# Performance work log

Measured on AMD Instinct MI355X. Metric: run time of the kernel, lower is better.

Reference implementation:

```python
import jax, jax.numpy as jnp
import numpy as np

S, B, I, H, O = 2048, 4096, 1, 8, 1  # seq_len, batch, input_size, hidden_size, output_size


def setup_inputs() -> dict:
    key = jax.random.key(0)
    ks = jax.random.split(key, 11)
    bound = 1.0 / np.sqrt(H)  # torch LSTMCell/Linear default init range

    def p(k, shape):
        return jax.random.uniform(k, shape, jnp.float32, -bound, bound)

    return {
        "x": jax.random.normal(ks[0], (S, B, I), jnp.float32),
        "w_ih_f": p(ks[1], (4 * H, I)),
        "w_hh_f": p(ks[2], (4 * H, H)),
        "b_ih_f": p(ks[3], (4 * H,)),
        "b_hh_f": p(ks[4], (4 * H,)),
        "w_ih_b": p(ks[5], (4 * H, I)),
        "w_hh_b": p(ks[6], (4 * H, H)),
        "b_ih_b": p(ks[7], (4 * H,)),
        "b_hh_b": p(ks[8], (4 * H,)),
        "w_out": p(ks[9], (O, 2 * H)),
        "b_out": p(ks[10], (O,)),
        "future": 0,
    }


def _lstm_scan(xseq, w_ih, w_hh, b_ih, b_hh):
    """Run an LSTMCell (torch gate order i,f,g,o) over [S,B,I]; returns h seq [S,B,H]."""
    Sq, Bq, _ = xseq.shape
    Hq = w_hh.shape[1]
    # hoist the input projection out of the recurrence: one big GEMM
    xg = jnp.einsum('sbi,gi->sbg', xseq, w_ih) + b_ih + b_hh  # [S,B,4H]

    def step(carry, xg_t):
        h, c = carry
        gates = xg_t + h @ w_hh.T  # [B,4H]
        i_g, f_g, g_g, o_g = jnp.split(gates, 4, axis=-1)
        i_g = jax.nn.sigmoid(i_g)
        f_g = jax.nn.sigmoid(f_g)
        g_g = jnp.tanh(g_g)
        o_g = jax.nn.sigmoid(o_g)
        c = f_g * c + i_g * g_g
        h = o_g * jnp.tanh(c)
        return (h, c), h

    h0 = jnp.zeros((Bq, Hq), xseq.dtype)
    _, hs = jax.lax.scan(step, (h0, h0), xg)
    return hs


def reference(x, w_ih_f, w_hh_f, b_ih_f, b_hh_f, w_ih_b, w_hh_b, b_ih_b, b_hh_b, w_out, b_out, future):
    Sq, Bq, _ = x.shape
    # forward direction reads x[i]
    hf = _lstm_scan(x, w_ih_f, w_hh_f, b_ih_f, b_hh_f)  # [S,B,H]
    # backward cell reads x[future - i]; with torch negative indexing this is (future - i) mod S
    idx = (future - jnp.arange(Sq)) % Sq
    hb = _lstm_scan(x[idx], w_ih_b, w_hh_b, b_ih_b, b_hh_b)  # [S,B,H]
    # outputs[i] = Linear(cat(h_f[i], h_b[i]))
    h = jnp.concatenate([hf, hb], axis=-1)  # [S,B,2H]
    out = jnp.einsum('sbh,oh->sbo', h, w_out) + b_out  # [S,B,O]
    # torch.cat(outputs, dim=1): step-major columns -> [B, S*O]
    return out.transpose(1, 0, 2).reshape(Bq, Sq * out.shape[-1])
```

## Files before the change

### kernel.cpp

```cpp
#include <hip/hip_runtime.h>

#define SLEN  2048
#define BATCH 4096

template<int CTRL>
__device__ __forceinline__ float dppf(float v) {
#if __has_builtin(__builtin_amdgcn_mov_dpp)
    return __int_as_float(
        __builtin_amdgcn_mov_dpp(__float_as_int(v), CTRL, 0xF, 0xF, true));
#else
    return __int_as_float(
        __builtin_amdgcn_update_dpp(0, __float_as_int(v), CTRL, 0xF, 0xF, true));
#endif
}
#define DPP_XOR1 0xB1
#define DPP_XOR2 0x4E
#define DPP_XOR3 0x1B
#define DPP_XOR7 0x141

__device__ __forceinline__ void pkfma_acc(float2& acc, float2 a, float2 b) {
    asm("v_pk_fma_f32 %0, %1, %2, %0" : "+v"(acc) : "v"(a), "v"(b));
}
template<int Q>
__device__ __forceinline__ void pkfma_bc(float2& acc, float2 h2, float2 w) {
    if constexpr (Q == 0)
        asm("v_pk_fma_f32 %0, %1, %2, %0 op_sel:[0,0,0] op_sel_hi:[0,1,1]"
            : "+v"(acc) : "v"(h2), "v"(w));
    else
        asm("v_pk_fma_f32 %0, %1, %2, %0 op_sel:[1,0,0] op_sel_hi:[1,1,1]"
            : "+v"(acc) : "v"(h2), "v"(w));
}

extern "C" __global__ __launch_bounds__(256, 1)
void bilstm_kernel(const float* __restrict__ x,
                   const float* __restrict__ w_ih_f, const float* __restrict__ w_hh_f,
                   const float* __restrict__ b_ih_f, const float* __restrict__ b_hh_f,
                   const float* __restrict__ w_ih_b, const float* __restrict__ w_hh_b,
                   const float* __restrict__ b_ih_b, const float* __restrict__ b_hh_b,
                   const float* __restrict__ w_out, const float* __restrict__ b_out,
                   const int* __restrict__ future_p,
                   float* __restrict__ out)
{
    const int tid  = threadIdx.x;
    const int wv   = tid >> 6;
    const int lane = tid & 63;
    const int e    = lane >> 4;
    const int r    = lane & 15;
    const int d    = r >> 3;
    const int j    = r & 7;
    const int b    = blockIdx.x * 16 + wv * 4 + e;

    const float* wih_p = d ? w_ih_b : w_ih_f;
    const float* whh_p = d ? w_hh_b : w_hh_f;
    const float* bih_p = d ? b_ih_b : b_ih_f;
    const float* bhh_p = d ? b_hh_b : b_hh_f;

    const float SI = -1.4426950408889634f;
    const float SG = -2.8853900817779268f;

    const int M[8] = {0, 1, 2, 3, 7, 6, 5, 4};
    float2 Wif[8], Wgo[8], wih_if, wih_go, b_if, b_go;
    #pragma unroll
    for (int m = 0; m < 8; ++m) {
        const int idx = j ^ M[m];
        Wif[m].x = SI * whh_p[(0 + j) * 8 + idx];
        Wif[m].y = SI * whh_p[(8 + j) * 8 + idx];
        Wgo[m].x = SG * whh_p[(16 + j) * 8 + idx];
        Wgo[m].y = SI * whh_p[(24 + j) * 8 + idx];
    }
    wih_if.x = SI * wih_p[0 + j];   wih_if.y = SI * wih_p[8 + j];
    wih_go.x = SG * wih_p[16 + j];  wih_go.y = SI * wih_p[24 + j];
    b_if.x = SI * (bih_p[0 + j]  + bhh_p[0 + j]);
    b_if.y = SI * (bih_p[8 + j]  + bhh_p[8 + j]);
    b_go.x = SG * (bih_p[16 + j] + bhh_p[16 + j]);
    b_go.y = SI * (bih_p[24 + j] + bhh_p[24 + j]);

    const float wout = w_out[d * 8 + j];
    const float bout = b_out[0];
    const int   fut  = future_p[0];

    __shared__ float o_lds[4][4][2][33];

    float c  = 0.0f;
    float hn = 0.0f;

    const char* xb = (const char*)x;
    unsigned voff = ((unsigned)(d ? (fut & (SLEN - 1)) : 0) * BATCH + (unsigned)b) * 4u;
    const unsigned vdelta = d ? (unsigned)(-(BATCH * 4)) : (unsigned)(BATCH * 4);
    const unsigned vmask  = (unsigned)(SLEN * BATCH * 4 - 1);

    float xv[8], xn[8];
    #pragma unroll
    for (int u = 0; u < 8; ++u) {
        xv[u] = *(const float*)(xb + voff);
        voff = (voff + vdelta) & vmask;
    }

    for (int t0 = 0; t0 < SLEN; t0 += 8) {
        const bool pf = (t0 + 8) < SLEN;
        if (pf) {
            #pragma unroll
            for (int u = 0; u < 8; ++u) {
                xn[u] = *(const float*)(xb + voff);
                voff = (voff + vdelta) & vmask;
            }
        }
        #pragma unroll
        for (int u = 0; u < 8; ++u) {
            float2 P0, P1, P2, P3;
            P0.x = hn;
            P0.y = dppf<DPP_XOR1>(hn);
            P1.x = dppf<DPP_XOR2>(hn);
            P1.y = dppf<DPP_XOR3>(hn);
            P2.x = dppf<DPP_XOR7>(P0.x);
            P2.y = dppf<DPP_XOR7>(P0.y);
            P3.x = dppf<DPP_XOR7>(P1.x);
            P3.y = dppf<DPP_XOR7>(P1.y);

            float2 xv2; xv2.x = xv[u]; xv2.y = xv[u];
            float2 acc_if = b_if, acc_go = b_go;
            pkfma_acc(acc_if, xv2, wih_if);
            pkfma_acc(acc_go, xv2, wih_go);
            pkfma_bc<0>(acc_if, P0, Wif[0]);  pkfma_bc<1>(acc_if, P0, Wif[1]);
            pkfma_bc<0>(acc_if, P1, Wif[2]);  pkfma_bc<1>(acc_if, P1, Wif[3]);
            pkfma_bc<0>(acc_if, P2, Wif[4]);  pkfma_bc<1>(acc_if, P2, Wif[5]);
            pkfma_bc<0>(acc_if, P3, Wif[6]);  pkfma_bc<1>(acc_if, P3, Wif[7]);
            pkfma_bc<0>(acc_go, P0, Wgo[0]);  pkfma_bc<1>(acc_go, P0, Wgo[1]);
            pkfma_bc<0>(acc_go, P1, Wgo[2]);  pkfma_bc<1>(acc_go, P1, Wgo[3]);
            pkfma_bc<0>(acc_go, P2, Wgo[4]);  pkfma_bc<1>(acc_go, P2, Wgo[5]);
            pkfma_bc<0>(acc_go, P3, Wgo[6]);  pkfma_bc<1>(acc_go, P3, Wgo[7]);

            float ia = __builtin_amdgcn_rcpf(1.0f + __builtin_amdgcn_exp2f(acc_if.x));
            float fa = __builtin_amdgcn_rcpf(1.0f + __builtin_amdgcn_exp2f(acc_if.y));
            float rg = __builtin_amdgcn_rcpf(1.0f + __builtin_amdgcn_exp2f(acc_go.x));
            float oa = __builtin_amdgcn_rcpf(1.0f + __builtin_amdgcn_exp2f(acc_go.y));
            float ga = fmaf(2.0f, rg, -1.0f);

            c = fmaf(fa, c, ia * ga);
            float tc = __builtin_amdgcn_exp2f(SG * c);
            float T  = fmaf(2.0f, __builtin_amdgcn_rcpf(1.0f + tc), -1.0f);
            hn = oa * T;

            float p = hn * wout;
            p += dppf<DPP_XOR1>(p);
            p += dppf<DPP_XOR2>(p);
            p += dppf<DPP_XOR7>(p);
            if ((r & 7) == 0) o_lds[wv][e][d][(t0 + u) & 31] = p;
        }
        if ((t0 & 31) == 24) {
            __builtin_amdgcn_wave_barrier();
            const int le = lane >> 4, lo = lane & 15;
            const int bb = blockIdx.x * 16 + wv * 4 + le;
            const int s0 = t0 - 24;
            float v0 = o_lds[wv][le][0][lo]      + o_lds[wv][le][1][lo];
            float v1 = o_lds[wv][le][0][lo + 16] + o_lds[wv][le][1][lo + 16];
            out[bb * SLEN + s0 + lo]      = v0 + bout;
            out[bb * SLEN + s0 + 16 + lo] = v1 + bout;
            __builtin_amdgcn_wave_barrier();
        }
        if (pf) {
            #pragma unroll
            for (int u = 0; u < 8; ++u) xv[u] = xn[u];
        }
    }
}

extern "C" void kernel_launch(void* const* d_in, const int* in_sizes, int n_in,
                              void* d_out, int out_size, void* d_ws, size_t ws_size,
                              hipStream_t stream) {
    const float* xp     = (const float*)d_in[0];
    const float* wihf   = (const float*)d_in[1];
    const float* whhf   = (const float*)d_in[2];
    const float* bihf   = (const float*)d_in[3];
    const float* bhhf   = (const float*)d_in[4];
    const float* wihb   = (const float*)d_in[5];
    const float* whhb   = (const float*)d_in[6];
    const float* bihb   = (const float*)d_in[7];
    const float* bhhb   = (const float*)d_in[8];
    const float* wo     = (const float*)d_in[9];
    const float* bo     = (const float*)d_in[10];
    const int*   futp   = (const int*)d_in[11];
    float*       outp   = (float*)d_out;

    dim3 grid(BATCH / 16);
    dim3 block(256);
    hipLaunchKernelGGL(bilstm_kernel, grid, block, 0, stream,
                       xp, wihf, whhf, bihf, bhhf, wihb, whhb, bihb, bhhb,
                       wo, bo, futp, outp);
}
```

Baseline: 340.8 us.

## Merge sigmoid reciprocals, branch-free LDS stores, packed x prefetch ring

```diff
diff --git a/kernel.cpp b/kernel.cpp
--- a/kernel.cpp
+++ b/kernel.cpp
@@ -5,21 +5,24 @@
 
 template<int CTRL>
 __device__ __forceinline__ float dppf(float v) {
-#if __has_builtin(__builtin_amdgcn_mov_dpp)
-    return __int_as_float(
-        __builtin_amdgcn_mov_dpp(__float_as_int(v), CTRL, 0xF, 0xF, true));
-#else
     return __int_as_float(
         __builtin_amdgcn_update_dpp(0, __float_as_int(v), CTRL, 0xF, 0xF, true));
-#endif
 }
 #define DPP_XOR1 0xB1
 #define DPP_XOR2 0x4E
 #define DPP_XOR3 0x1B
 #define DPP_XOR7 0x141
 
-__device__ __forceinline__ void pkfma_acc(float2& acc, float2 a, float2 b) {
-    asm("v_pk_fma_f32 %0, %1, %2, %0" : "+v"(acc) : "v"(a), "v"(b));
+template<int Q>
+__device__ __forceinline__ float2 pkfma_init(float2 x2, float2 w, float2 b) {
+    float2 dst;
+    if constexpr (Q == 0)
+        asm("v_pk_fma_f32 %0, %1, %2, %3 op_sel:[0,0,0] op_sel_hi:[0,1,1]"
+            : "=v"(dst) : "v"(x2), "v"(w), "v"(b));
+    else
+        asm("v_pk_fma_f32 %0, %1, %2, %3 op_sel:[1,0,0] op_sel_hi:[1,1,1]"
+            : "=v"(dst) : "v"(x2), "v"(w), "v"(b));
+    return dst;
 }
 template<int Q>
 __device__ __forceinline__ void pkfma_bc(float2& acc, float2 h2, float2 w) {
@@ -79,7 +82,9 @@
     const float bout = b_out[0];
     const int   fut  = future_p[0];
 
-    __shared__ float o_lds[4][4][2][33];
+    __shared__ float o_lds[4][8][72];
+    float* o_ptr = &o_lds[wv][e * 2 + d][(j == 0) ? 0 : (32 + j)];
+    float* o_base = &o_lds[wv][0][0];
 
     float c  = 0.0f;
     float hn = 0.0f;
@@ -89,79 +94,88 @@
     const unsigned vdelta = d ? (unsigned)(-(BATCH * 4)) : (unsigned)(BATCH * 4);
     const unsigned vmask  = (unsigned)(SLEN * BATCH * 4 - 1);
 
-    float xv[8], xn[8];
+    float2 xa2[4], xb2[4];
     #pragma unroll
-    for (int u = 0; u < 8; ++u) {
-        xv[u] = *(const float*)(xb + voff);
-        voff = (voff + vdelta) & vmask;
+    for (int p = 0; p < 4; ++p) {
+        xa2[p].x = *(const float*)(xb + voff); voff = (voff + vdelta) & vmask;
+        xa2[p].y = *(const float*)(xb + voff); voff = (voff + vdelta) & vmask;
     }
 
-    for (int t0 = 0; t0 < SLEN; t0 += 8) {
-        const bool pf = (t0 + 8) < SLEN;
-        if (pf) {
+    auto STEP = [&](float2 acc_if, float2 acc_go, int slot) {
+        float2 P0, P1, P2, P3;
+        P0.x = hn;
+        P0.y = dppf<DPP_XOR1>(hn);
+        P1.x = dppf<DPP_XOR2>(hn);
+        P1.y = dppf<DPP_XOR3>(hn);
+        P2.x = dppf<DPP_XOR7>(P0.x);
+        P2.y = dppf<DPP_XOR7>(P0.y);
+        P3.x = dppf<DPP_XOR7>(P1.x);
+        P3.y = dppf<DPP_XOR7>(P1.y);
+
+        pkfma_bc<0>(acc_if, P0, Wif[0]);  pkfma_bc<1>(acc_if, P0, Wif[1]);
+        pkfma_bc<0>(acc_if, P1, Wif[2]);  pkfma_bc<1>(acc_if, P1, Wif[3]);
+        pkfma_bc<0>(acc_if, P2, Wif[4]);  pkfma_bc<1>(acc_if, P2, Wif[5]);
+        pkfma_bc<0>(acc_if, P3, Wif[6]);  pkfma_bc<1>(acc_if, P3, Wif[7]);
+        pkfma_bc<0>(acc_go, P0, Wgo[0]);  pkfma_bc<1>(acc_go, P0, Wgo[1]);
+        pkfma_bc<0>(acc_go, P1, Wgo[2]);  pkfma_bc<1>(acc_go, P1, Wgo[3]);
+        pkfma_bc<0>(acc_go, P2, Wgo[4]);  pkfma_bc<1>(acc_go, P2, Wgo[5]);
+        pkfma_bc<0>(acc_go, P3, Wgo[6]);  pkfma_bc<1>(acc_go, P3, Wgo[7]);
+
+        float ei = __builtin_amdgcn_exp2f(acc_if.x);
+        float ef = __builtin_amdgcn_exp2f(acc_if.y);
+        float eg = __builtin_amdgcn_exp2f(acc_go.x);
+        float eo = __builtin_amdgcn_exp2f(acc_go.y);
+        float ei1 = 1.0f + ei, ef1 = 1.0f + ef, eg1 = 1.0f + eg, eo1 = 1.0f + eo;
+        float riu = __builtin_amdgcn_rcpf(ei1 * eg1);
+        float ig  = (2.0f - eg1) * riu;
+        float rv  = __builtin_amdgcn_rcpf(ef1 * eo1);
+        float fa  = rv * eo1;
+        float oa  = rv * ef1;
+        c = fmaf(fa, c, ig);
+        float tc = __builtin_amdgcn_exp2f(SG * c);
+        float rt = __builtin_amdgcn_rcpf(1.0f + tc);
+        float T  = fmaf(2.0f, rt, -1.0f);
+        hn = oa * T;
+
+        float p = hn * wout;
+        p += dppf<DPP_XOR1>(p);
+        p += dppf<DPP_XOR2>(p);
+        p += dppf<DPP_XOR7>(p);
+        o_ptr[slot] = p;
+    };
+
+    for (int T = 0; T < SLEN; T += 32) {
+        #pragma unroll
+        for (int blk = 0; blk < 4; ++blk) {
             #pragma unroll
-            for (int u = 0; u < 8; ++u) {
-                xn[u] = *(const float*)(xb + voff);
-                voff = (voff + vdelta) & vmask;
+            for (int p = 0; p < 4; ++p) {
+                if (blk & 1) {
+                    xa2[p].x = *(const float*)(xb + voff); voff = (voff + vdelta) & vmask;
+                    xa2[p].y = *(const float*)(xb + voff); voff = (voff + vdelta) & vmask;
+                } else {
+                    xb2[p].x = *(const float*)(xb + voff); voff = (voff + vdelta) & vmask;
+                    xb2[p].y = *(const float*)(xb + voff); voff = (voff + vdelta) & vmask;
+                }
+            }
+            #pragma unroll
+            for (int p = 0; p < 4; ++p) {
+                float2 x2 = (blk & 1) ? xb2[p] : xa2[p];
+                STEP(pkfma_init<0>(x2, wih_if, b_if),
+                     pkfma_init<0>(x2, wih_go, b_go), blk * 8 + 2 * p);
+                STEP(pkfma_init<1>(x2, wih_if, b_if),
+                     pkfma_init<1>(x2, wih_go, b_go), blk * 8 + 2 * p + 1);
             }
         }
-        #pragma unroll
-        for (int u = 0; u < 8; ++u) {
-            float2 P0, P1, P2, P3;
-            P0.x = hn;
-            P0.y = dppf<DPP_XOR1>(hn);
-            P1.x = dppf<DPP_XOR2>(hn);
-            P1.y = dppf<DPP_XOR3>(hn);
-            P2.x = dppf<DPP_XOR7>(P0.x);
-            P2.y = dppf<DPP_XOR7>(P0.y);
-            P3.x = dppf<DPP_XOR7>(P1.x);
-            P3.y = dppf<DPP_XOR7>(P1.y);
-
-            float2 xv2; xv2.x = xv[u]; xv2.y = xv[u];
-            float2 acc_if = b_if, acc_go = b_go;
-            pkfma_acc(acc_if, xv2, wih_if);
-            pkfma_acc(acc_go, xv2, wih_go);
-            pkfma_bc<0>(acc_if, P0, Wif[0]);  pkfma_bc<1>(acc_if, P0, Wif[1]);
-            pkfma_bc<0>(acc_if, P1, Wif[2]);  pkfma_bc<1>(acc_if, P1, Wif[3]);
-            pkfma_bc<0>(acc_if, P2, Wif[4]);  pkfma_bc<1>(acc_if, P2, Wif[5]);
-            pkfma_bc<0>(acc_if, P3, Wif[6]);  pkfma_bc<1>(acc_if, P3, Wif[7]);
-            pkfma_bc<0>(acc_go, P0, Wgo[0]);  pkfma_bc<1>(acc_go, P0, Wgo[1]);
-            pkfma_bc<0>(acc_go, P1, Wgo[2]);  pkfma_bc<1>(acc_go, P1, Wgo[3]);
-            pkfma_bc<0>(acc_go, P2, Wgo[4]);  pkfma_bc<1>(acc_go, P2, Wgo[5]);
-            pkfma_bc<0>(acc_go, P3, Wgo[6]);  pkfma_bc<1>(acc_go, P3, Wgo[7]);
-
-            float ia = __builtin_amdgcn_rcpf(1.0f + __builtin_amdgcn_exp2f(acc_if.x));
-            float fa = __builtin_amdgcn_rcpf(1.0f + __builtin_amdgcn_exp2f(acc_if.y));
-            float rg = __builtin_amdgcn_rcpf(1.0f + __builtin_amdgcn_exp2f(acc_go.x));
-            float oa = __builtin_amdgcn_rcpf(1.0f + __builtin_amdgcn_exp2f(acc_go.y));
-            float ga = fmaf(2.0f, rg, -1.0f);
-
-            c = fmaf(fa, c, ia * ga);
-            float tc = __builtin_amdgcn_exp2f(SG * c);
-            float T  = fmaf(2.0f, __builtin_amdgcn_rcpf(1.0f + tc), -1.0f);
-            hn = oa * T;
-
-            float p = hn * wout;
-            p += dppf<DPP_XOR1>(p);
-            p += dppf<DPP_XOR2>(p);
-            p += dppf<DPP_XOR7>(p);
-            if ((r & 7) == 0) o_lds[wv][e][d][(t0 + u) & 31] = p;
-        }
-        if ((t0 & 31) == 24) {
-            __builtin_amdgcn_wave_barrier();
+        __builtin_amdgcn_wave_barrier();
+        {
             const int le = lane >> 4, lo = lane & 15;
             const int bb = blockIdx.x * 16 + wv * 4 + le;
-            const int s0 = t0 - 24;
-            float v0 = o_lds[wv][le][0][lo]      + o_lds[wv][le][1][lo];
-            float v1 = o_lds[wv][le][0][lo + 16] + o_lds[wv][le][1][lo + 16];
-            out[bb * SLEN + s0 + lo]      = v0 + bout;
-            out[bb * SLEN + s0 + 16 + lo] = v1 + bout;
-            __builtin_amdgcn_wave_barrier();
+            float v0 = o_base[(le * 2 + 0) * 72 + lo]      + o_base[(le * 2 + 1) * 72 + lo];
+            float v1 = o_base[(le * 2 + 0) * 72 + lo + 16] + o_base[(le * 2 + 1) * 72 + lo + 16];
+            out[bb * SLEN + T + lo]      = v0 + bout;
+            out[bb * SLEN + T + 16 + lo] = v1 + bout;
         }
-        if (pf) {
-            #pragma unroll
-            for (int u = 0; u < 8; ++u) xv[u] = xn[u];
-        }
+        __builtin_amdgcn_wave_barrier();
     }
 }
 
```

Measured after the change: 297.8 us. 1.14x faster.
